# Kernel tuning notes

Hardware: AMD Instinct MI355X
Metric: run time of the kernel (lower is better)

Reference implementation:

```python
import math
import jax, jax.numpy as jnp
import numpy as np

D_MODEL = 1024
HEADS = 16
B, S = 4, 2048


def setup_inputs() -> dict:
    key = jax.random.key(0)
    ks = jax.random.split(key, 8)
    scale = 1.0 / math.sqrt(D_MODEL)
    return {
        "q": jax.random.normal(ks[0], (B, S, D_MODEL), dtype=jnp.float32),
        "k": jax.random.normal(ks[1], (B, S, D_MODEL), dtype=jnp.float32),
        "v": jax.random.normal(ks[2], (B, S, D_MODEL), dtype=jnp.float32),
        "mask": jax.random.randint(ks[3], (B, S), 0, 2).astype(jnp.bool_),
        "alibi_mask": jax.random.normal(ks[4], (1, HEADS, S, S), dtype=jnp.float32),
        "Wq": jax.random.normal(ks[5], (D_MODEL, D_MODEL), dtype=jnp.float32) * scale,
        "Wk": jax.random.normal(ks[6], (D_MODEL, D_MODEL), dtype=jnp.float32) * scale,
        "Wv": jax.random.normal(ks[7], (D_MODEL, D_MODEL), dtype=jnp.float32) * scale,
    }


def _split_heads(x):
    b, s, d = x.shape
    return x.reshape(b, s, HEADS, d // HEADS).transpose(0, 2, 1, 3)  # [B,H,S,hd]


def reference(q, k, v, mask, alibi_mask, Wq, Wk, Wv):
    # QKV projections (Linear, no bias)
    qh = _split_heads(q @ Wq)
    kh = _split_heads(k @ Wk)
    vh = _split_heads(v @ Wv)
    depth = qh.shape[-1]
    # naive full attention matrix [B,H,Sq,Sk]
    w = jnp.einsum("bhqd,bhkd->bhqk", qh, kh) / math.sqrt(depth)
    # mask: [B,Sk] -> [B,1,1,Sk], True = masked
    w = jnp.where(mask[:, None, None, :], -jnp.inf, w)
    w = w + alibi_mask
    a = jax.nn.softmax(w, axis=-1)  # dropout p=0 -> identity
    out = jnp.einsum("bhqk,bhkd->bhqd", a, vh)
    # combine heads -> [B,S,D]
    out = out.transpose(0, 2, 1, 3).reshape(q.shape[0], q.shape[1], -1)
    return (out, a)
```

## Files before the change

kernel.cpp:

```cpp
#include <hip/hip_runtime.h>
#include <hip/hip_bf16.h>
#include <math.h>

constexpr int B  = 4;
constexpr int S  = 2048;
constexpr int D  = 1024;
constexpr int H  = 16;
constexpr int HD = 64;
constexpr float LOG2E  = 1.4426950408889634f;
constexpr float SCALE2 = 0.125f * LOG2E;

using f32x4 = __attribute__((ext_vector_type(4))) float;
using s16x8 = __attribute__((ext_vector_type(8))) short;
using u16x8 = __attribute__((ext_vector_type(8))) unsigned short;
using u16x4 = __attribute__((ext_vector_type(4))) unsigned short;

__device__ __forceinline__ unsigned short f2bf(float f) {
    union { float f; unsigned u; } x; x.f = f;
    unsigned r = x.u + 0x7fffu + ((x.u >> 16) & 1u);
    return (unsigned short)(r >> 16);
}
__device__ __forceinline__ unsigned short f2bf_fast(float f) {
    union { float f; unsigned u; } x; x.f = f;
    return (unsigned short)((x.u + 0x8000u) >> 16);
}
__device__ __forceinline__ float bf2f(unsigned short h) {
    union { unsigned u; float f; } x; x.u = ((unsigned)h) << 16;
    return x.f;
}
__device__ __forceinline__ float fexp2(float x) {
#if __has_builtin(__builtin_amdgcn_exp2f)
    return __builtin_amdgcn_exp2f(x);
#else
    return __expf(x * 0.6931471805599453f);
#endif
}

#define MFMA_BF16(Af, Bf, Cf) __builtin_amdgcn_mfma_f32_16x16x32_bf16(Af, Bf, Cf, 0, 0, 0)

__global__ __launch_bounds__(256) void k_prep(
    const float* __restrict__ Xq, const float* __restrict__ Xk,
    const float* __restrict__ Xv,
    unsigned short* __restrict__ qb, unsigned short* __restrict__ kb,
    unsigned short* __restrict__ vb,
    const float* __restrict__ Wq, const float* __restrict__ Wk,
    const float* __restrict__ Wv,
    unsigned short* __restrict__ wqt, unsigned short* __restrict__ wkt,
    unsigned short* __restrict__ wvt,
    const float* __restrict__ ALIBI, unsigned short* __restrict__ ABF,
    int do_abf) {
    __shared__ unsigned short T[64][68];
    const int bid = blockIdx.x;
    const int t = threadIdx.x;

    if (bid < 6144) {
        const int op = bid >> 11, xb = bid & 2047;
        const float* X = op == 0 ? Xq : (op == 1 ? Xk : Xv);
        unsigned short* O = op == 0 ? qb : (op == 1 ? kb : vb);
        const size_t N = (size_t)B * S * D;
        const size_t stride = (size_t)2048 * 256 * 8;
        for (size_t i = ((size_t)xb * 256 + t) * 8; i < N; i += stride) {
            f32x4 a0 = __builtin_nontemporal_load(reinterpret_cast<const f32x4*>(&X[i]));
            f32x4 a1 = __builtin_nontemporal_load(reinterpret_cast<const f32x4*>(&X[i + 4]));
            u16x8 o;
#pragma unroll
            for (int j = 0; j < 4; ++j) { o[j] = f2bf(a0[j]); o[4 + j] = f2bf(a1[j]); }
            *reinterpret_cast<u16x8*>(&O[i]) = o;
        }
    } else if (bid < 6912) {
        const int idx = bid - 6144;
        const int op = idx >> 8, r = idx & 255;
        const float* W = op == 0 ? Wq : (op == 1 ? Wk : Wv);
        unsigned short* Wt = op == 0 ? wqt : (op == 1 ? wkt : wvt);
        const int k0 = (r & 15) * 64, n0 = (r >> 4) * 64;
        {
            const int kr = t >> 4, nc4 = (t & 15) * 4;
            for (int rr = 0; rr < 4; ++rr) {
                const int kk = kr + rr * 16;
                f32x4 wv = __builtin_nontemporal_load(
                    reinterpret_cast<const f32x4*>(&W[(size_t)(k0 + kk) * D + n0 + nc4]));
#pragma unroll
                for (int j = 0; j < 4; ++j) T[nc4 + j][kk] = f2bf(wv[j]);
            }
        }
        __syncthreads();
        {
            const int nr = t >> 4, kc4 = (t & 15) * 4;
            for (int rr = 0; rr < 4; ++rr) {
                const int nn = nr + rr * 16;
                u16x4 o;
#pragma unroll
                for (int j = 0; j < 4; ++j) o[j] = T[nn][kc4 + j];
                *reinterpret_cast<u16x4*>(&Wt[(size_t)(n0 + nn) * D + k0 + kc4]) = o;
            }
        }
    } else {
        if (!do_abf) return;
        const int idx = bid - 6912;
        const size_t N = (size_t)H * S * S;
        const size_t stride = (size_t)8192 * 256 * 8;
        for (size_t i = ((size_t)idx * 256 + t) * 8; i < N; i += stride) {
            f32x4 a0 = __builtin_nontemporal_load(reinterpret_cast<const f32x4*>(&ALIBI[i]));
            f32x4 a1 = __builtin_nontemporal_load(reinterpret_cast<const f32x4*>(&ALIBI[i + 4]));
            u16x8 o;
#pragma unroll
            for (int j = 0; j < 4; ++j) {
                o[j]     = f2bf(a0[j] * LOG2E);
                o[4 + j] = f2bf(a1[j] * LOG2E);
            }
            *reinterpret_cast<u16x8*>(&ABF[i]) = o;
        }
    }
}

__global__ __launch_bounds__(256) void k_proj2(const unsigned short* __restrict__ Xq,
                                               const unsigned short* __restrict__ Xk,
                                               const unsigned short* __restrict__ wqt,
                                               const unsigned short* __restrict__ wkt,
                                               unsigned short* __restrict__ qh,
                                               unsigned short* __restrict__ kh) {
    const unsigned short* X = blockIdx.z == 0 ? Xq : Xk;
    const unsigned short* Wt = blockIdx.z == 0 ? wqt : wkt;
    unsigned short* Y = blockIdx.z == 0 ? qh : kh;

    __shared__ alignas(16) unsigned short As[128][72];
    __shared__ alignas(16) unsigned short Bs[128][72];
    const int bm = blockIdx.y * 128, bn = blockIdx.x * 128;
    const int t = threadIdx.x, w = t >> 6, l = t & 63;
    const int wr = w >> 1, wc = w & 1;
    const int lr = l & 15, lg = l >> 4;
    f32x4 acc[4][4] = {};

    for (int k0 = 0; k0 < D; k0 += 64) {
        for (int i = 0; i < 4; ++i) {
            const int idx = t + i * 256;
            const int row = idx >> 3, c8 = (idx & 7) * 8;
            *reinterpret_cast<u16x8*>(&As[row][c8]) =
                *reinterpret_cast<const u16x8*>(&X[(size_t)(bm + row) * D + k0 + c8]);
            *reinterpret_cast<u16x8*>(&Bs[row][c8]) =
                *reinterpret_cast<const u16x8*>(&Wt[(size_t)(bn + row) * D + k0 + c8]);
        }
        __syncthreads();
#pragma unroll
        for (int kk = 0; kk < 2; ++kk) {
            s16x8 af[4], bf[4];
#pragma unroll
            for (int f = 0; f < 4; ++f) {
                af[f] = *reinterpret_cast<const s16x8*>(&As[wr * 64 + f * 16 + lr][kk * 32 + lg * 8]);
                bf[f] = *reinterpret_cast<const s16x8*>(&Bs[wc * 64 + f * 16 + lr][kk * 32 + lg * 8]);
            }
#pragma unroll
            for (int fm = 0; fm < 4; ++fm)
#pragma unroll
                for (int fn = 0; fn < 4; ++fn)
                    acc[fm][fn] = MFMA_BF16(af[fm], bf[fn], acc[fm][fn]);
        }
        __syncthreads();
    }
#pragma unroll
    for (int fm = 0; fm < 4; ++fm)
#pragma unroll
        for (int fn = 0; fn < 4; ++fn)
#pragma unroll
            for (int r = 0; r < 4; ++r) {
                const int m = bm + wr * 64 + fm * 16 + lg * 4 + r;
                const int n = bn + wc * 64 + fn * 16 + lr;
                const int b = m >> 11, s = m & (S - 1);
                const int h = n >> 6, e = n & 63;
                Y[(((size_t)(b * H + h) * S) + s) * HD + e] = f2bf(acc[fm][fn][r]);
            }
}

__global__ __launch_bounds__(256) void k_projv_mfma(const unsigned short* __restrict__ X,
                                                    const unsigned short* __restrict__ Wt,
                                                    unsigned short* __restrict__ VT) {
    __shared__ alignas(16) unsigned short SM[2][128][72];
    unsigned short (*As)[72] = SM[0];
    unsigned short (*Bs)[72] = SM[1];
    const int bm = blockIdx.y * 128, bn = blockIdx.x * 128;
    const int t = threadIdx.x, w = t >> 6, l = t & 63;
    const int wr = w >> 1, wc = w & 1;
    const int lr = l & 15, lg = l >> 4;
    f32x4 acc[4][4] = {};

    for (int k0 = 0; k0 < D; k0 += 64) {
        for (int i = 0; i < 4; ++i) {
            const int idx = t + i * 256;
            const int row = idx >> 3, c8 = (idx & 7) * 8;
            *reinterpret_cast<u16x8*>(&As[row][c8]) =
                *reinterpret_cast<const u16x8*>(&X[(size_t)(bm + row) * D + k0 + c8]);
            *reinterpret_cast<u16x8*>(&Bs[row][c8]) =
                *reinterpret_cast<const u16x8*>(&Wt[(size_t)(bn + row) * D + k0 + c8]);
        }
        __syncthreads();
#pragma unroll
        for (int kk = 0; kk < 2; ++kk) {
            s16x8 af[4], bf[4];
#pragma unroll
            for (int f = 0; f < 4; ++f) {
                af[f] = *reinterpret_cast<const s16x8*>(&As[wr * 64 + f * 16 + lr][kk * 32 + lg * 8]);
                bf[f] = *reinterpret_cast<const s16x8*>(&Bs[wc * 64 + f * 16 + lr][kk * 32 + lg * 8]);
            }
#pragma unroll
            for (int fm = 0; fm < 4; ++fm)
#pragma unroll
                for (int fn = 0; fn < 4; ++fn)
                    acc[fm][fn] = MFMA_BF16(af[fm], bf[fn], acc[fm][fn]);
        }
        __syncthreads();
    }
    unsigned short (*T)[144] = reinterpret_cast<unsigned short(*)[144]>(&SM[0][0][0]);
#pragma unroll
    for (int fm = 0; fm < 4; ++fm)
#pragma unroll
        for (int fn = 0; fn < 4; ++fn)
#pragma unroll
            for (int r = 0; r < 4; ++r)
                T[wc * 64 + fn * 16 + lr][wr * 64 + fm * 16 + lg * 4 + r] = f2bf(acc[fm][fn][r]);
    __syncthreads();
    const int b = bm >> 11, s0 = bm & (S - 1);
    for (int it = 0; it < 8; ++it) {
        const int idx = t + it * 256;
        const int row = idx >> 4, c8 = (idx & 15) * 8;
        const int h = (bn + row) >> 6, e = (bn + row) & 63;
        *reinterpret_cast<u16x8*>(&VT[((size_t)(b * H + h) * HD + e) * S + s0 + c8]) =
            *reinterpret_cast<const u16x8*>(&T[row][c8]);
    }
}

template <bool ABF16>
__global__ __launch_bounds__(512, 4) void k_sumexp(
    const unsigned short* __restrict__ QH, const unsigned short* __restrict__ KH,
    const float* __restrict__ ALIBI, const unsigned short* __restrict__ ABF,
    const int* __restrict__ MASK, float* __restrict__ INVL) {
    __shared__ alignas(16) unsigned short Ks[64][72];
    __shared__ alignas(16) unsigned short ALs[128][72];

    const int bid = blockIdx.x;
    const int wg = (bid & 7) * 128 + (bid >> 3);
    const int bh = wg >> 4, b = bh >> 4, h = bh & 15;
    const int q0 = (wg & 15) * 128;
    const int t = threadIdx.x, w = t >> 6, ln = t & 63;
    const int lr = ln & 15, lg = ln >> 4;
    const unsigned short NEGBIG = f2bf(-1e30f);
    const size_t hoff = (size_t)h * S * S;

    const unsigned short* Kb = KH + (size_t)bh * S * HD;

    s16x8 qf[2];
#pragma unroll
    for (int kk = 0; kk < 2; ++kk)
        qf[kk] = *reinterpret_cast<const s16x8*>(
            &QH[((size_t)bh * S + q0 + w * 16 + lr) * HD + kk * 32 + lg * 8]);

    float psum = 0.f;

    for (int k0 = 0; k0 < S; k0 += 64) {
        {
            const int row = t >> 3, c8 = (t & 7) * 8;
            *reinterpret_cast<u16x8*>(&Ks[row][c8]) =
                *reinterpret_cast<const u16x8*>(&Kb[(size_t)(k0 + row) * HD + c8]);
        }
#pragma unroll
        for (int i = 0; i < 2; ++i) {
            const int idx = t + i * 512, row = idx >> 3, c8 = (idx & 7) * 8;
            int4 m0 = *reinterpret_cast<const int4*>(&MASK[b * S + k0 + c8]);
            int4 m1 = *reinterpret_cast<const int4*>(&MASK[b * S + k0 + c8 + 4]);
            u16x8 av;
            if constexpr (ABF16) {
                av = *reinterpret_cast<const u16x8*>(&ABF[hoff + (size_t)(q0 + row) * S + k0 + c8]);
            } else {
                f32x4 a0 = *reinterpret_cast<const f32x4*>(&ALIBI[hoff + (size_t)(q0 + row) * S + k0 + c8]);
                f32x4 a1 = *reinterpret_cast<const f32x4*>(&ALIBI[hoff + (size_t)(q0 + row) * S + k0 + c8 + 4]);
#pragma unroll
                for (int j = 0; j < 4; ++j) {
                    av[j] = f2bf(a0[j] * LOG2E);
                    av[4 + j] = f2bf(a1[j] * LOG2E);
                }
            }
            u16x8 sv;
            sv[0] = m0.x ? NEGBIG : av[0];
            sv[1] = m0.y ? NEGBIG : av[1];
            sv[2] = m0.z ? NEGBIG : av[2];
            sv[3] = m0.w ? NEGBIG : av[3];
            sv[4] = m1.x ? NEGBIG : av[4];
            sv[5] = m1.y ? NEGBIG : av[5];
            sv[6] = m1.z ? NEGBIG : av[6];
            sv[7] = m1.w ? NEGBIG : av[7];
            *reinterpret_cast<u16x8*>(&ALs[row][c8]) = sv;
        }
        __syncthreads();

        f32x4 acc[4] = {};
#pragma unroll
        for (int kk = 0; kk < 2; ++kk)
#pragma unroll
            for (int fn = 0; fn < 4; ++fn) {
                s16x8 kf = *reinterpret_cast<const s16x8*>(&Ks[fn * 16 + lr][kk * 32 + lg * 8]);
                acc[fn] = MFMA_BF16(kf, qf[kk], acc[fn]);
            }
#pragma unroll
        for (int fn = 0; fn < 4; ++fn) {
            u16x4 alv = *reinterpret_cast<const u16x4*>(&ALs[w * 16 + lr][fn * 16 + lg * 4]);
            f32x4 al;
#pragma unroll
            for (int j = 0; j < 4; ++j) al[j] = bf2f(alv[j]);
            f32x4 sv = acc[fn] * SCALE2 + al;
            psum += fexp2(sv[0]) + fexp2(sv[1]) + fexp2(sv[2]) + fexp2(sv[3]);
        }
        __syncthreads();
    }

    psum += __shfl_xor(psum, 16, 64);
    psum += __shfl_xor(psum, 32, 64);
    if (lg == 0)
        INVL[(size_t)bh * S + q0 + w * 16 + lr] = 1.0f / psum;
}

template <bool ABF16>
__global__ __launch_bounds__(512, 4) void k_attn(
    const unsigned short* __restrict__ QH, const unsigned short* __restrict__ KH,
    const unsigned short* __restrict__ VT, const float* __restrict__ ALIBI,
    const unsigned short* __restrict__ ABF, const int* __restrict__ MASK,
    const float* __restrict__ INVL, float* __restrict__ Aout,
    float* __restrict__ OUT) {
    __shared__ alignas(16) unsigned short Ks[64][72];
    __shared__ alignas(16) unsigned short Vs[64][72];
    __shared__ alignas(16) unsigned short ALs[128][72];

    const int bid = blockIdx.x;
    const int wg = (bid & 7) * 128 + (bid >> 3);
    const int bh = wg >> 4, b = bh >> 4, h = bh & 15;
    const int q0 = (wg & 15) * 128;
    const int t = threadIdx.x, w = t >> 6, ln = t & 63;
    const int lr = ln & 15, lg = ln >> 4;
    const unsigned short NEGBIG = f2bf(-1e30f);
    const size_t hoff = (size_t)h * S * S;

    const unsigned short* Kb = KH + (size_t)bh * S * HD;
    const unsigned short* Vb = VT + (size_t)bh * HD * S;

    s16x8 qf[2];
#pragma unroll
    for (int kk = 0; kk < 2; ++kk)
        qf[kk] = *reinterpret_cast<const s16x8*>(
            &QH[((size_t)bh * S + q0 + w * 16 + lr) * HD + kk * 32 + lg * 8]);

    const float invl = INVL[(size_t)bh * S + q0 + w * 16 + lr];
    float* arow = Aout + ((size_t)bh * S + q0 + w * 16 + lr) * S;

    f32x4 oacc[4] = {};

    for (int k0 = 0; k0 < S; k0 += 64) {
        {
            const int row = t >> 3, c8 = (t & 7) * 8;
            *reinterpret_cast<u16x8*>(&Ks[row][c8]) =
                *reinterpret_cast<const u16x8*>(&Kb[(size_t)(k0 + row) * HD + c8]);
            *reinterpret_cast<u16x8*>(&Vs[row][c8]) =
                *reinterpret_cast<const u16x8*>(&Vb[(size_t)row * S + k0 + c8]);
        }
#pragma unroll
        for (int i = 0; i < 2; ++i) {
            const int idx = t + i * 512, row = idx >> 3, c8 = (idx & 7) * 8;
            int4 m0 = *reinterpret_cast<const int4*>(&MASK[b * S + k0 + c8]);
            int4 m1 = *reinterpret_cast<const int4*>(&MASK[b * S + k0 + c8 + 4]);
            u16x8 av;
            if constexpr (ABF16) {
                av = *reinterpret_cast<const u16x8*>(&ABF[hoff + (size_t)(q0 + row) * S + k0 + c8]);
            } else {
                f32x4 a0 = *reinterpret_cast<const f32x4*>(&ALIBI[hoff + (size_t)(q0 + row) * S + k0 + c8]);
                f32x4 a1 = *reinterpret_cast<const f32x4*>(&ALIBI[hoff + (size_t)(q0 + row) * S + k0 + c8 + 4]);
#pragma unroll
                for (int j = 0; j < 4; ++j) {
                    av[j] = f2bf(a0[j] * LOG2E);
                    av[4 + j] = f2bf(a1[j] * LOG2E);
                }
            }
            u16x8 sv;
            sv[0] = m0.x ? NEGBIG : av[0];
            sv[1] = m0.y ? NEGBIG : av[1];
            sv[2] = m0.z ? NEGBIG : av[2];
            sv[3] = m0.w ? NEGBIG : av[3];
            sv[4] = m1.x ? NEGBIG : av[4];
            sv[5] = m1.y ? NEGBIG : av[5];
            sv[6] = m1.z ? NEGBIG : av[6];
            sv[7] = m1.w ? NEGBIG : av[7];
            *reinterpret_cast<u16x8*>(&ALs[row][c8]) = sv;
        }
        __syncthreads();

        f32x4 acc[4] = {};
#pragma unroll
        for (int kk = 0; kk < 2; ++kk)
#pragma unroll
            for (int fn = 0; fn < 4; ++fn) {
                s16x8 kf = *reinterpret_cast<const s16x8*>(&Ks[fn * 16 + lr][kk * 32 + lg * 8]);
                acc[fn] = MFMA_BF16(kf, qf[kk], acc[fn]);
            }

#pragma unroll
        for (int fn = 0; fn < 4; ++fn) {
            u16x4 alv = *reinterpret_cast<const u16x4*>(&ALs[w * 16 + lr][fn * 16 + lg * 4]);
            f32x4 al;
#pragma unroll
            for (int j = 0; j < 4; ++j) al[j] = bf2f(alv[j]);
            f32x4 sv = acc[fn] * SCALE2 + al;
            f32x4 p;
#pragma unroll
            for (int j = 0; j < 4; ++j) p[j] = fexp2(sv[j]);
            p *= invl;
            __builtin_nontemporal_store(
                p, reinterpret_cast<f32x4*>(arow + k0 + fn * 16 + lg * 4));
            u16x4 pb;
#pragma unroll
            for (int j = 0; j < 4; ++j) pb[j] = f2bf_fast(p[j]);
            *reinterpret_cast<u16x4*>(&ALs[w * 16 + lr][fn * 16 + lg * 4]) = pb;
        }

#pragma unroll
        for (int c = 0; c < 2; ++c) {
            s16x8 pa = *reinterpret_cast<const s16x8*>(&ALs[w * 16 + lr][c * 32 + lg * 8]);
#pragma unroll
            for (int fn = 0; fn < 4; ++fn) {
                s16x8 vf = *reinterpret_cast<const s16x8*>(&Vs[fn * 16 + lr][c * 32 + lg * 8]);
                oacc[fn] = MFMA_BF16(pa, vf, oacc[fn]);
            }
        }
        __syncthreads();
    }

#pragma unroll
    for (int fn = 0; fn < 4; ++fn)
#pragma unroll
        for (int r = 0; r < 4; ++r)
            OUT[(size_t)(b * S + q0 + w * 16 + lg * 4 + r) * D + h * HD + fn * 16 + lr] =
                oacc[fn][r];
}

extern "C" void kernel_launch(void* const* d_in, const int* in_sizes, int n_in,
                              void* d_out, int out_size, void* d_ws, size_t ws_size,
                              hipStream_t stream) {
    const float* q     = (const float*)d_in[0];
    const float* k     = (const float*)d_in[1];
    const float* v     = (const float*)d_in[2];
    const int*   mask  = (const int*)d_in[3];
    const float* alibi = (const float*)d_in[4];
    const float* Wq    = (const float*)d_in[5];
    const float* Wk    = (const float*)d_in[6];
    const float* Wv    = (const float*)d_in[7];

    float* out = (float*)d_out;
    float* a   = out + (size_t)B * S * D;

    const size_t NH = (size_t)B * H * S * HD;
    unsigned short* qh  = (unsigned short*)d_ws;
    unsigned short* kh  = qh + NH;
    unsigned short* vT  = kh + NH;
    unsigned short* wqt = vT + NH;
    unsigned short* wkt = wqt + (size_t)D * D;
    unsigned short* wvt = wkt + (size_t)D * D;
    unsigned short* qb  = wvt + (size_t)D * D;
    unsigned short* kb  = qb + NH;
    unsigned short* vb  = kb + NH;
    float*          invl = (float*)(vb + NH);
    unsigned short* abf  = (unsigned short*)(invl + (size_t)B * H * S);

    const size_t need_bf16 =
        ((size_t)(abf - qh) + (size_t)H * S * S) * sizeof(unsigned short);
    const bool use_abf16 = ws_size >= need_bf16;

    const dim3 blk(256);

    k_prep<<<dim3(15104), blk, 0, stream>>>(q, k, v, qb, kb, vb,
                                            Wq, Wk, Wv, wqt, wkt, wvt,
                                            alibi, abf, use_abf16 ? 1 : 0);

    k_proj2<<<dim3(D / 128, (B * S) / 128, 2), blk, 0, stream>>>(qb, kb, wqt, wkt, qh, kh);
    k_projv_mfma<<<dim3(D / 128, (B * S) / 128), blk, 0, stream>>>(vb, wvt, vT);

    if (use_abf16) {
        k_sumexp<true><<<dim3(1024), dim3(512), 0, stream>>>(
            qh, kh, alibi, abf, mask, invl);
        k_attn<true><<<dim3(1024), dim3(512), 0, stream>>>(
            qh, kh, vT, alibi, abf, mask, invl, a, out);
    } else {
        k_sumexp<false><<<dim3(1024), dim3(512), 0, stream>>>(
            qh, kh, alibi, abf, mask, invl);
        k_attn<false><<<dim3(1024), dim3(512), 0, stream>>>(
            qh, kh, vT, alibi, abf, mask, invl, a, out);
    }
}
```

Baseline: 599.4 us.

## Co-schedule QKV projection GEMMs with alibi bf16 conversion in one kernel

Moves the alibi fp32-to-bf16 conversion out of the prep kernel and merges it with the Q/K/V projection GEMMs into a single launch. Blocks are interleaved 3 GEMM tiles to 8 conversion blocks out of every 11, so the compute-bound MFMA work overlaps the bandwidth-bound alibi streaming. It also saves one launch by merging the separate V projection kernel. The risk is that the blocks compete for bandwidth and LDS, and that conversion blocks now reserve the GEMM's larger shared memory, which lowers their occupancy.

```diff
diff --git a/kernel.cpp b/kernel.cpp
--- a/kernel.cpp
+++ b/kernel.cpp
@@ -46,9 +46,7 @@
     const float* __restrict__ Wq, const float* __restrict__ Wk,
     const float* __restrict__ Wv,
     unsigned short* __restrict__ wqt, unsigned short* __restrict__ wkt,
-    unsigned short* __restrict__ wvt,
-    const float* __restrict__ ALIBI, unsigned short* __restrict__ ABF,
-    int do_abf) {
+    unsigned short* __restrict__ wvt) {
     __shared__ unsigned short T[64][68];
     const int bid = blockIdx.x;
     const int t = threadIdx.x;
@@ -67,7 +65,7 @@
             for (int j = 0; j < 4; ++j) { o[j] = f2bf(a0[j]); o[4 + j] = f2bf(a1[j]); }
             *reinterpret_cast<u16x8*>(&O[i]) = o;
         }
-    } else if (bid < 6912) {
+    } else {
         const int idx = bid - 6144;
         const int op = idx >> 8, r = idx & 255;
         const float* W = op == 0 ? Wq : (op == 1 ? Wk : Wv);
@@ -94,12 +92,104 @@
                 *reinterpret_cast<u16x4*>(&Wt[(size_t)(n0 + nn) * D + k0 + kc4]) = o;
             }
         }
+    }
+}
+
+__global__ __launch_bounds__(256) void k_projabf(
+    const unsigned short* __restrict__ qb, const unsigned short* __restrict__ kb,
+    const unsigned short* __restrict__ vb,
+    const unsigned short* __restrict__ wqt, const unsigned short* __restrict__ wkt,
+    const unsigned short* __restrict__ wvt,
+    unsigned short* __restrict__ qh, unsigned short* __restrict__ kh,
+    unsigned short* __restrict__ vT,
+    const float* __restrict__ ALIBI, unsigned short* __restrict__ ABF,
+    int do_abf) {
+    __shared__ alignas(16) unsigned short SM[2][128][72];
+    const int bid = blockIdx.x;
+    const int t = threadIdx.x;
+    const int sel = bid % 11;
+
+    if (sel < 3) {
+        const int pidx = (bid / 11) * 3 + sel;
+        const int op = pidx >> 10;
+        const int r  = pidx & 1023;
+        const int bn = (r & 7) * 128, bm = (r >> 3) * 128;
+        const unsigned short* X  = op == 0 ? qb : (op == 1 ? kb : vb);
+        const unsigned short* Wt = op == 0 ? wqt : (op == 1 ? wkt : wvt);
+        unsigned short (*As)[72] = SM[0];
+        unsigned short (*Bs)[72] = SM[1];
+        const int w = t >> 6, l = t & 63;
+        const int wr = w >> 1, wc = w & 1;
+        const int lr = l & 15, lg = l >> 4;
+        f32x4 acc[4][4] = {};
+
+        for (int k0 = 0; k0 < D; k0 += 64) {
+            for (int i = 0; i < 4; ++i) {
+                const int idx = t + i * 256;
+                const int row = idx >> 3, c8 = (idx & 7) * 8;
+                *reinterpret_cast<u16x8*>(&As[row][c8]) =
+                    *reinterpret_cast<const u16x8*>(&X[(size_t)(bm + row) * D + k0 + c8]);
+                *reinterpret_cast<u16x8*>(&Bs[row][c8]) =
+                    *reinterpret_cast<const u16x8*>(&Wt[(size_t)(bn + row) * D + k0 + c8]);
+            }
+            __syncthreads();
+#pragma unroll
+            for (int kk = 0; kk < 2; ++kk) {
+                s16x8 af[4], bf[4];
+#pragma unroll
+                for (int f = 0; f < 4; ++f) {
+                    af[f] = *reinterpret_cast<const s16x8*>(&As[wr * 64 + f * 16 + lr][kk * 32 + lg * 8]);
+                    bf[f] = *reinterpret_cast<const s16x8*>(&Bs[wc * 64 + f * 16 + lr][kk * 32 + lg * 8]);
+                }
+#pragma unroll
+                for (int fm = 0; fm < 4; ++fm)
+#pragma unroll
+                    for (int fn = 0; fn < 4; ++fn)
+                        acc[fm][fn] = MFMA_BF16(af[fm], bf[fn], acc[fm][fn]);
+            }
+            __syncthreads();
+        }
+
+        if (op < 2) {
+            unsigned short* Y = op == 0 ? qh : kh;
+#pragma unroll
+            for (int fm = 0; fm < 4; ++fm)
+#pragma unroll
+                for (int fn = 0; fn < 4; ++fn)
+#pragma unroll
+                    for (int rr = 0; rr < 4; ++rr) {
+                        const int m = bm + wr * 64 + fm * 16 + lg * 4 + rr;
+                        const int n = bn + wc * 64 + fn * 16 + lr;
+                        const int b = m >> 11, s = m & (S - 1);
+                        const int h = n >> 6, e = n & 63;
+                        Y[(((size_t)(b * H + h) * S) + s) * HD + e] = f2bf(acc[fm][fn][rr]);
+                    }
+        } else {
+            unsigned short (*T)[144] = reinterpret_cast<unsigned short(*)[144]>(&SM[0][0][0]);
+#pragma unroll
+            for (int fm = 0; fm < 4; ++fm)
+#pragma unroll
+                for (int fn = 0; fn < 4; ++fn)
+#pragma unroll
+                    for (int rr = 0; rr < 4; ++rr)
+                        T[wc * 64 + fn * 16 + lr][wr * 64 + fm * 16 + lg * 4 + rr] =
+                            f2bf(acc[fm][fn][rr]);
+            __syncthreads();
+            const int b = bm >> 11, s0 = bm & (S - 1);
+            for (int it = 0; it < 8; ++it) {
+                const int idx = t + it * 256;
+                const int row = idx >> 4, c8 = (idx & 15) * 8;
+                const int h = (bn + row) >> 6, e = (bn + row) & 63;
+                *reinterpret_cast<u16x8*>(&vT[((size_t)(b * H + h) * HD + e) * S + s0 + c8]) =
+                    *reinterpret_cast<const u16x8*>(&T[row][c8]);
+            }
+        }
     } else {
         if (!do_abf) return;
-        const int idx = bid - 6912;
+        const int aidx = (bid / 11) * 8 + (sel - 3);
         const size_t N = (size_t)H * S * S;
         const size_t stride = (size_t)8192 * 256 * 8;
-        for (size_t i = ((size_t)idx * 256 + t) * 8; i < N; i += stride) {
+        for (size_t i = ((size_t)aidx * 256 + t) * 8; i < N; i += stride) {
             f32x4 a0 = __builtin_nontemporal_load(reinterpret_cast<const f32x4*>(&ALIBI[i]));
             f32x4 a1 = __builtin_nontemporal_load(reinterpret_cast<const f32x4*>(&ALIBI[i + 4]));
             u16x8 o;
@@ -110,121 +200,6 @@
             }
             *reinterpret_cast<u16x8*>(&ABF[i]) = o;
         }
-    }
-}
-
-__global__ __launch_bounds__(256) void k_proj2(const unsigned short* __restrict__ Xq,
-                                               const unsigned short* __restrict__ Xk,
-                                               const unsigned short* __restrict__ wqt,
-                                               const unsigned short* __restrict__ wkt,
-                                               unsigned short* __restrict__ qh,
-                                               unsigned short* __restrict__ kh) {
-    const unsigned short* X = blockIdx.z == 0 ? Xq : Xk;
-    const unsigned short* Wt = blockIdx.z == 0 ? wqt : wkt;
-    unsigned short* Y = blockIdx.z == 0 ? qh : kh;
-
-    __shared__ alignas(16) unsigned short As[128][72];
-    __shared__ alignas(16) unsigned short Bs[128][72];
-    const int bm = blockIdx.y * 128, bn = blockIdx.x * 128;
-    const int t = threadIdx.x, w = t >> 6, l = t & 63;
-    const int wr = w >> 1, wc = w & 1;
-    const int lr = l & 15, lg = l >> 4;
-    f32x4 acc[4][4] = {};
-
-    for (int k0 = 0; k0 < D; k0 += 64) {
-        for (int i = 0; i < 4; ++i) {
-            const int idx = t + i * 256;
-            const int row = idx >> 3, c8 = (idx & 7) * 8;
-            *reinterpret_cast<u16x8*>(&As[row][c8]) =
-                *reinterpret_cast<const u16x8*>(&X[(size_t)(bm + row) * D + k0 + c8]);
-            *reinterpret_cast<u16x8*>(&Bs[row][c8]) =
-                *reinterpret_cast<const u16x8*>(&Wt[(size_t)(bn + row) * D + k0 + c8]);
-        }
-        __syncthreads();
-#pragma unroll
-        for (int kk = 0; kk < 2; ++kk) {
-            s16x8 af[4], bf[4];
-#pragma unroll
-            for (int f = 0; f < 4; ++f) {
-                af[f] = *reinterpret_cast<const s16x8*>(&As[wr * 64 + f * 16 + lr][kk * 32 + lg * 8]);
-                bf[f] = *reinterpret_cast<const s16x8*>(&Bs[wc * 64 + f * 16 + lr][kk * 32 + lg * 8]);
-            }
-#pragma unroll
-            for (int fm = 0; fm < 4; ++fm)
-#pragma unroll
-                for (int fn = 0; fn < 4; ++fn)
-                    acc[fm][fn] = MFMA_BF16(af[fm], bf[fn], acc[fm][fn]);
-        }
-        __syncthreads();
-    }
-#pragma unroll
-    for (int fm = 0; fm < 4; ++fm)
-#pragma unroll
-        for (int fn = 0; fn < 4; ++fn)
-#pragma unroll
-            for (int r = 0; r < 4; ++r) {
-                const int m = bm + wr * 64 + fm * 16 + lg * 4 + r;
-                const int n = bn + wc * 64 + fn * 16 + lr;
-                const int b = m >> 11, s = m & (S - 1);
-                const int h = n >> 6, e = n & 63;
-                Y[(((size_t)(b * H + h) * S) + s) * HD + e] = f2bf(acc[fm][fn][r]);
-            }
-}
-
-__global__ __launch_bounds__(256) void k_projv_mfma(const unsigned short* __restrict__ X,
-                                                    const unsigned short* __restrict__ Wt,
-                                                    unsigned short* __restrict__ VT) {
-    __shared__ alignas(16) unsigned short SM[2][128][72];
-    unsigned short (*As)[72] = SM[0];
-    unsigned short (*Bs)[72] = SM[1];
-    const int bm = blockIdx.y * 128, bn = blockIdx.x * 128;
-    const int t = threadIdx.x, w = t >> 6, l = t & 63;
-    const int wr = w >> 1, wc = w & 1;
-    const int lr = l & 15, lg = l >> 4;
-    f32x4 acc[4][4] = {};
-
-    for (int k0 = 0; k0 < D; k0 += 64) {
-        for (int i = 0; i < 4; ++i) {
-            const int idx = t + i * 256;
-            const int row = idx >> 3, c8 = (idx & 7) * 8;
-            *reinterpret_cast<u16x8*>(&As[row][c8]) =
-                *reinterpret_cast<const u16x8*>(&X[(size_t)(bm + row) * D + k0 + c8]);
-            *reinterpret_cast<u16x8*>(&Bs[row][c8]) =
-                *reinterpret_cast<const u16x8*>(&Wt[(size_t)(bn + row) * D + k0 + c8]);
-        }
-        __syncthreads();
-#pragma unroll
-        for (int kk = 0; kk < 2; ++kk) {
-            s16x8 af[4], bf[4];
-#pragma unroll
-            for (int f = 0; f < 4; ++f) {
-                af[f] = *reinterpret_cast<const s16x8*>(&As[wr * 64 + f * 16 + lr][kk * 32 + lg * 8]);
-                bf[f] = *reinterpret_cast<const s16x8*>(&Bs[wc * 64 + f * 16 + lr][kk * 32 + lg * 8]);
-            }
-#pragma unroll
-            for (int fm = 0; fm < 4; ++fm)
-#pragma unroll
-                for (int fn = 0; fn < 4; ++fn)
-                    acc[fm][fn] = MFMA_BF16(af[fm], bf[fn], acc[fm][fn]);
-        }
-        __syncthreads();
-    }
-    unsigned short (*T)[144] = reinterpret_cast<unsigned short(*)[144]>(&SM[0][0][0]);
-#pragma unroll
-    for (int fm = 0; fm < 4; ++fm)
-#pragma unroll
-        for (int fn = 0; fn < 4; ++fn)
-#pragma unroll
-            for (int r = 0; r < 4; ++r)
-                T[wc * 64 + fn * 16 + lr][wr * 64 + fm * 16 + lg * 4 + r] = f2bf(acc[fm][fn][r]);
-    __syncthreads();
-    const int b = bm >> 11, s0 = bm & (S - 1);
-    for (int it = 0; it < 8; ++it) {
-        const int idx = t + it * 256;
-        const int row = idx >> 4, c8 = (idx & 15) * 8;
-        const int h = (bn + row) >> 6, e = (bn + row) & 63;
-        *reinterpret_cast<u16x8*>(&VT[((size_t)(b * H + h) * HD + e) * S + s0 + c8]) =
-            *reinterpret_cast<const u16x8*>(&T[row][c8]);
     }
 }
 
@@ -471,12 +446,12 @@
 
     const dim3 blk(256);
 
-    k_prep<<<dim3(15104), blk, 0, stream>>>(q, k, v, qb, kb, vb,
-                                            Wq, Wk, Wv, wqt, wkt, wvt,
-                                            alibi, abf, use_abf16 ? 1 : 0);
-
-    k_proj2<<<dim3(D / 128, (B * S) / 128, 2), blk, 0, stream>>>(qb, kb, wqt, wkt, qh, kh);
-    k_projv_mfma<<<dim3(D / 128, (B * S) / 128), blk, 0, stream>>>(vb, wvt, vT);
+    k_prep<<<dim3(6912), blk, 0, stream>>>(q, k, v, qb, kb, vb,
+                                           Wq, Wk, Wv, wqt, wkt, wvt);
+
+    k_projabf<<<dim3(11264), blk, 0, stream>>>(qb, kb, vb, wqt, wkt, wvt,
+                                               qh, kh, vT, alibi, abf,
+                                               use_abf16 ? 1 : 0);
 
     if (use_abf16) {
         k_sumexp<true><<<dim3(1024), dim3(512), 0, stream>>>(
```

Result: slower. 683.7 us (+14.1%).
